# Kernel optimization log

Hardware: AMD Instinct MI355X
Metric: run time of the kernel (lower is better)

## Reference

```python
import jax, jax.numpy as jnp
import numpy as np

N, E, FN, FE, L, G = 4096, 16384, 16, 8, 128, 64
EPS = 1e-5


def setup_inputs() -> dict:
    key = jax.random.key(0)
    ks = iter(jax.random.split(key, 40))

    def lin_w(shape):
        return jax.random.normal(next(ks), shape, jnp.float32) * (1.0 / np.sqrt(shape[0]))

    d = {}
    d["x"] = jax.random.normal(next(ks), (N, FN), jnp.float32)
    d["edge_attr"] = jax.random.normal(next(ks), (E, FE), jnp.float32)
    d["edge_index"] = jax.random.randint(next(ks), (2, E), 0, N)
    d["batch"] = jnp.sort(jax.random.randint(next(ks), (N,), 0, G))
    for i, (cin, cout) in enumerate([(FN, 32), (32, 64), (64, 128)], 1):
        d[f"We{i}"] = lin_w((FE, cin * cout))          # edge_fc weight
        d[f"be{i}"] = jnp.zeros((cin * cout,), jnp.float32)
        d[f"bias{i}"] = jnp.zeros((cout,), jnp.float32)
        d[f"Wr{i}"] = lin_w((cin, cout))               # res_fc weight
        d[f"br{i}"] = jnp.zeros((cout,), jnp.float32)
        d[f"bn_g{i}"] = jnp.ones((cout,), jnp.float32)
        d[f"bn_b{i}"] = jnp.zeros((cout,), jnp.float32)
        d[f"a{i}"] = jnp.float32(0.25)                  # PReLU slope
    d["Wi"] = lin_w((128, 128)); d["bi"] = jnp.zeros((128,), jnp.float32)
    d["Wj"] = lin_w((128, 128)); d["bj"] = jnp.zeros((128,), jnp.float32)
    d["Wfc"] = lin_w((128, 2 * L)); d["bfc"] = jnp.zeros((2 * L,), jnp.float32)
    return d


def _ecc(x, src, dst, norm, edge_attr, We, be, bias, Wr, br, cout, cin):
    # dynamically generated per-edge filter: [E, out, in]
    theta = (edge_attr @ We + be).reshape(E, cout, cin)
    # gather source features, per-edge matvec, degree-normalize (norm_j)
    msg = norm[src][:, None] * jnp.einsum('eoi,ei->eo', theta, x[src])
    # scatter-add into destination nodes + bias + residual linear
    return jax.ops.segment_sum(msg, dst, num_segments=N) + bias + x @ Wr + br


def _bn(x, g, b):
    m = x.mean(0)
    v = x.var(0)  # biased variance, as torch BN training normalization
    return (x - m) * jax.lax.rsqrt(v + EPS) * g + b


def _prelu(x, a):
    return jnp.where(x >= 0, x, a * x)


def reference(x, edge_attr, edge_index, batch,
              We1, be1, bias1, Wr1, br1, bn_g1, bn_b1, a1,
              We2, be2, bias2, Wr2, br2, bn_g2, bn_b2, a2,
              We3, be3, bias3, Wr3, br3, bn_g3, bn_b3, a3,
              Wi, bi, Wj, bj, Wfc, bfc):
    src, dst = edge_index[0], edge_index[1]
    deg = jax.ops.segment_sum(jnp.ones((E,), x.dtype), src, num_segments=N)
    norm = jnp.where(deg > 0, 1.0 / deg, 0.0)

    h = _ecc(x, src, dst, norm, edge_attr, We1, be1, bias1, Wr1, br1, 32, FN)
    h = _prelu(_bn(h, bn_g1, bn_b1), a1)
    h = _ecc(h, src, dst, norm, edge_attr, We2, be2, bias2, Wr2, br2, 64, 32)
    h = _prelu(_bn(h, bn_g2, bn_b2), a2)
    h = _ecc(h, src, dst, norm, edge_attr, We3, be3, bias3, Wr3, br3, 128, 64)
    h = _prelu(_bn(h, bn_g3, bn_b3), a3)

    # gated attention pooling (GGS-NN eq. 7), scatter-sum per graph
    gates = jax.nn.sigmoid(h @ Wi + bi)
    feats = jnp.tanh(h @ Wj + bj)
    pooled = jnp.tanh(jax.ops.segment_sum(gates * feats, batch, num_segments=G))

    z = pooled @ Wfc + bfc  # [G, 2L]
    return z[:, :L], z[:, L:]
```

## Files before the change

kernel.cpp:

```cpp
#include <hip/hip_runtime.h>
#include <math.h>

#define NN 4096
#define NE 16384
#define NG 64

#define OFF_DEG   0
#define OFF_H1    4096
#define OFF_H2    135168
#define OFF_H3    397312
#define OFF_ST1   921600
#define OFF_ST2   921664
#define OFF_ST3   921792
#define OFF_POOL  922048
#define OFF_WC1   930240
#define OFF_WC2   934848
#define OFF_WC3   953280
#define OFF_Y     1027008
#define ZERO_FLOATS 930240

__device__ __forceinline__ void tr_wcat(const float* We, const float* be,
                                        float* Wcat, int CIN, int COUT, int t) {
    int nine = 9 * COUT;
    int i = t / nine; int r = t - i * nine;
    int f = r / COUT; int o = r - f * COUT;
    Wcat[t] = (f < 8) ? We[f * CIN * COUT + o * CIN + i] : be[o * CIN + i];
}

__global__ __launch_bounds__(256) void k_prep(
    const float* __restrict__ We1, const float* __restrict__ be1,
    const float* __restrict__ We2, const float* __restrict__ be2,
    const float* __restrict__ We3, const float* __restrict__ be3,
    const int* __restrict__ ei, float* __restrict__ ws)
{
    int t = blockIdx.x * 256 + threadIdx.x;
    if (t < 4608)  { tr_wcat(We1, be1, ws + OFF_WC1, 16, 32, t); return; }
    t -= 4608;
    if (t < 18432) { tr_wcat(We2, be2, ws + OFF_WC2, 32, 64, t); return; }
    t -= 18432;
    if (t < 73728) { tr_wcat(We3, be3, ws + OFF_WC3, 64, 128, t); return; }
    t -= 73728;
    if (t < NE)    { atomicAdd(&ws[OFF_DEG + ei[t]], 1.0f); }
}

template<int K>
__global__ __launch_bounds__(256) void k_proj(
    const float* __restrict__ A,
    const float* __restrict__ B,
    const float* __restrict__ deg,
    float* __restrict__ Y, int Ncols)
{
    __shared__ float sA[K][68];
    __shared__ float sB[K][68];
    const int tid = threadIdx.x;
    const int m0 = blockIdx.x * 64;
    const int n0 = blockIdx.y * 64;

    for (int t = tid; t < 64 * K; t += 256) {
        int m = t / K, i = t - m * K;
        sA[i][m] = A[(m0 + m) * K + i];
    }
    for (int t = tid; t < 64 * K; t += 256) {
        int i = t / 64, n = t - i * 64;
        int col = n0 + n;
        sB[i][n] = (col < Ncols) ? B[i * Ncols + col] : 0.f;
    }
    __syncthreads();

    const int tn = tid % 16, tm = tid / 16;
    float acc[4][4] = {{0.f}};
#pragma unroll 8
    for (int i = 0; i < K; ++i) {
        float4 a = *(const float4*)&sA[i][tm * 4];
        float4 b = *(const float4*)&sB[i][tn * 4];
        acc[0][0] += a.x * b.x; acc[0][1] += a.x * b.y; acc[0][2] += a.x * b.z; acc[0][3] += a.x * b.w;
        acc[1][0] += a.y * b.x; acc[1][1] += a.y * b.y; acc[1][2] += a.y * b.z; acc[1][3] += a.y * b.w;
        acc[2][0] += a.z * b.x; acc[2][1] += a.z * b.y; acc[2][2] += a.z * b.z; acc[2][3] += a.z * b.w;
        acc[3][0] += a.w * b.x; acc[3][1] += a.w * b.y; acc[3][2] += a.w * b.z; acc[3][3] += a.w * b.w;
    }

#pragma unroll
    for (int mm = 0; mm < 4; ++mm) {
        int m = m0 + tm * 4 + mm;
        float d = deg[m];
        float nrm = d > 0.f ? 1.f / d : 0.f;
#pragma unroll
        for (int nn = 0; nn < 4; ++nn) {
            int col = n0 + tn * 4 + nn;
            if (col < Ncols) Y[(size_t)m * Ncols + col] = acc[mm][nn] * nrm;
        }
    }
}

template<int COUT>
__global__ __launch_bounds__(256) void k_egather(
    const float* __restrict__ Y, const float* __restrict__ eattr,
    const int* __restrict__ ei, float* __restrict__ h)
{
    int idx = blockIdx.x * 256 + threadIdx.x;
    int e = idx / COUT;
    int o = idx - e * COUT;
    int src = ei[e], dst = ei[NE + e];
    const float* y = Y + (size_t)src * (9 * COUT);
    const float* ea = eattr + e * 8;
    float acc = y[8 * COUT + o];
#pragma unroll
    for (int f = 0; f < 8; ++f) acc += ea[f] * y[f * COUT + o];
    atomicAdd(&h[dst * COUT + o], acc);
}

template<int CIN, int COUT, int KN>
__global__ __launch_bounds__(256) void k_node(
    const float* __restrict__ xin, const float* __restrict__ Wr,
    const float* __restrict__ br, const float* __restrict__ bias,
    float* __restrict__ h, float* __restrict__ st)
{
    constexpr int NL = 256 / COUT;
    constexpr int NB = NL * KN;
    constexpr int CINP = CIN | 1;
    __shared__ float sWr[CIN * COUT];
    __shared__ float sX[NB * CINP];
    __shared__ float sred[256];
    const int tid = threadIdx.x;
    const int nbase = blockIdx.x * NB;

    for (int t = tid; t < CIN * COUT; t += 256) sWr[t] = Wr[t];
    for (int t = tid; t < NB * CIN; t += 256) {
        int r = t / CIN, i = t - r * CIN;
        sX[r * CINP + i] = xin[(nbase + r) * CIN + i];
    }
    __syncthreads();

    const int o = tid % COUT;
    const int nl = tid / COUT;
    const float addc = bias[o] + br[o];
    float sum = 0.f, sumsq = 0.f;
    for (int k = 0; k < KN; ++k) {
        int r = nl * KN + k;
        float a = addc;
        for (int i = 0; i < CIN; ++i)
            a += sX[r * CINP + i] * sWr[i * COUT + o];
        int gi = (nbase + r) * COUT + o;
        float hv = h[gi] + a;
        h[gi] = hv;
        sum += hv; sumsq += hv * hv;
    }
    sred[tid] = sum;
    __syncthreads();
    if (tid < COUT) {
        float s = 0.f;
        for (int g2 = 0; g2 < NL; ++g2) s += sred[g2 * COUT + tid];
        atomicAdd(&st[tid], s);
    }
    __syncthreads();
    sred[tid] = sumsq;
    __syncthreads();
    if (tid < COUT) {
        float s = 0.f;
        for (int g2 = 0; g2 < NL; ++g2) s += sred[g2 * COUT + tid];
        atomicAdd(&st[COUT + tid], s);
    }
}

template<int COUT>
__global__ __launch_bounds__(256) void k_bn(
    float* __restrict__ h, const float* __restrict__ st,
    const float* __restrict__ g, const float* __restrict__ b,
    const float* __restrict__ a)
{
    int idx = blockIdx.x * 256 + threadIdx.x;
    int o = idx % COUT;
    float mean = st[o] * (1.f / NN);
    float var = st[COUT + o] * (1.f / NN) - mean * mean;
    var = fmaxf(var, 0.f);
    float inv = rsqrtf(var + 1e-5f);
    float v = (h[idx] - mean) * inv * g[o] + b[o];
    h[idx] = v >= 0.f ? v : a[0] * v;
}

__global__ __launch_bounds__(256) void k_pool(
    const float* __restrict__ h3, const int* __restrict__ batch,
    const float* __restrict__ Wi, const float* __restrict__ bi,
    const float* __restrict__ Wj, const float* __restrict__ bj,
    float* __restrict__ pooled)
{
    constexpr int KN = 8, NB = 16;
    __shared__ float sH[NB * 128];
    __shared__ int sB[NB];
    const int tid = threadIdx.x;
    const int nbase = blockIdx.x * NB;
    for (int t = tid; t < NB * 128; t += 256) sH[t] = h3[nbase * 128 + t];
    if (tid < NB) sB[tid] = batch[nbase + tid];
    __syncthreads();

    const int o = tid % 128, nl = tid / 128;
    float gacc[KN], facc[KN];
#pragma unroll
    for (int k = 0; k < KN; ++k) { gacc[k] = 0.f; facc[k] = 0.f; }
    for (int i = 0; i < 128; ++i) {
        float wi = Wi[i * 128 + o], wj = Wj[i * 128 + o];
#pragma unroll
        for (int k = 0; k < KN; ++k) {
            float hv = sH[(nl * KN + k) * 128 + i];
            gacc[k] += hv * wi;
            facc[k] += hv * wj;
        }
    }
    float bio = bi[o], bjo = bj[o];
#pragma unroll
    for (int k = 0; k < KN; ++k) {
        int r = nl * KN + k;
        float gate = 1.f / (1.f + expf(-(gacc[k] + bio)));
        float feat = tanhf(facc[k] + bjo);
        atomicAdd(&pooled[sB[r] * 128 + o], gate * feat);
    }
}

__global__ __launch_bounds__(256) void k_final(
    const float* __restrict__ pooled, const float* __restrict__ Wfc,
    const float* __restrict__ bfc, float* __restrict__ out)
{
    __shared__ float sP[128];
    const int g = blockIdx.x, c = threadIdx.x;
    if (c < 128) sP[c] = tanhf(pooled[g * 128 + c]);
    __syncthreads();
    float z = bfc[c];
    for (int i = 0; i < 128; ++i) z += sP[i] * Wfc[i * 256 + c];
    int oidx = (c < 128) ? (g * 128 + c) : (NG * 128 + g * 128 + (c - 128));
    out[oidx] = z;
}

extern "C" void kernel_launch(void* const* d_in, const int* in_sizes, int n_in,
                              void* d_out, int out_size, void* d_ws, size_t ws_size,
                              hipStream_t stream)
{
    (void)in_sizes; (void)n_in; (void)out_size; (void)ws_size;
    const float* x     = (const float*)d_in[0];
    const float* eattr = (const float*)d_in[1];
    const int*   ei    = (const int*)d_in[2];
    const int*   batch = (const int*)d_in[3];
    const float* We1 = (const float*)d_in[4];
    const float* be1 = (const float*)d_in[5];
    const float* bias1 = (const float*)d_in[6];
    const float* Wr1 = (const float*)d_in[7];
    const float* br1 = (const float*)d_in[8];
    const float* bg1 = (const float*)d_in[9];
    const float* bb1 = (const float*)d_in[10];
    const float* a1  = (const float*)d_in[11];
    const float* We2 = (const float*)d_in[12];
    const float* be2 = (const float*)d_in[13];
    const float* bias2 = (const float*)d_in[14];
    const float* Wr2 = (const float*)d_in[15];
    const float* br2 = (const float*)d_in[16];
    const float* bg2 = (const float*)d_in[17];
    const float* bb2 = (const float*)d_in[18];
    const float* a2  = (const float*)d_in[19];
    const float* We3 = (const float*)d_in[20];
    const float* be3 = (const float*)d_in[21];
    const float* bias3 = (const float*)d_in[22];
    const float* Wr3 = (const float*)d_in[23];
    const float* br3 = (const float*)d_in[24];
    const float* bg3 = (const float*)d_in[25];
    const float* bb3 = (const float*)d_in[26];
    const float* a3  = (const float*)d_in[27];
    const float* Wi  = (const float*)d_in[28];
    const float* bi  = (const float*)d_in[29];
    const float* Wj  = (const float*)d_in[30];
    const float* bj  = (const float*)d_in[31];
    const float* Wfc = (const float*)d_in[32];
    const float* bfc = (const float*)d_in[33];
    float* ws  = (float*)d_ws;
    float* out = (float*)d_out;

    hipMemsetAsync(d_ws, 0, (size_t)ZERO_FLOATS * sizeof(float), stream);
    k_prep<<<442, 256, 0, stream>>>(We1, be1, We2, be2, We3, be3, ei, ws);

    k_proj<16><<<dim3(64, 5), 256, 0, stream>>>(x, ws + OFF_WC1, ws + OFF_DEG, ws + OFF_Y, 288);
    k_egather<32><<<NE * 32 / 256, 256, 0, stream>>>(ws + OFF_Y, eattr, ei, ws + OFF_H1);
    k_node<16, 32, 8><<<NN / 64, 256, 0, stream>>>(x, Wr1, br1, bias1, ws + OFF_H1, ws + OFF_ST1);
    k_bn<32><<<NN * 32 / 256, 256, 0, stream>>>(ws + OFF_H1, ws + OFF_ST1, bg1, bb1, a1);

    k_proj<32><<<dim3(64, 9), 256, 0, stream>>>(ws + OFF_H1, ws + OFF_WC2, ws + OFF_DEG, ws + OFF_Y, 576);
    k_egather<64><<<NE * 64 / 256, 256, 0, stream>>>(ws + OFF_Y, eattr, ei, ws + OFF_H2);
    k_node<32, 64, 8><<<NN / 32, 256, 0, stream>>>(ws + OFF_H1, Wr2, br2, bias2, ws + OFF_H2, ws + OFF_ST2);
    k_bn<64><<<NN * 64 / 256, 256, 0, stream>>>(ws + OFF_H2, ws + OFF_ST2, bg2, bb2, a2);

    k_proj<64><<<dim3(64, 18), 256, 0, stream>>>(ws + OFF_H2, ws + OFF_WC3, ws + OFF_DEG, ws + OFF_Y, 1152);
    k_egather<128><<<NE * 128 / 256, 256, 0, stream>>>(ws + OFF_Y, eattr, ei, ws + OFF_H3);
    k_node<64, 128, 8><<<NN / 16, 256, 0, stream>>>(ws + OFF_H2, Wr3, br3, bias3, ws + OFF_H3, ws + OFF_ST3);
    k_bn<128><<<NN * 128 / 256, 256, 0, stream>>>(ws + OFF_H3, ws + OFF_ST3, bg3, bb3, a3);

    k_pool<<<NN / 16, 256, 0, stream>>>(ws + OFF_H3, batch, Wi, bi, Wj, bj, ws + OFF_POOL);
    k_final<<<NG, 256, 0, stream>>>(ws + OFF_POOL, Wfc, bfc, out);
}
```

Before: 255.9 us.

## Fold residual linear into projection GEMM and fuse BN+PReLU into consumers

Appends the residual weight Wr as extra columns of the per-layer projection GEMM, so h is initialised with x@Wr+bias+br before edge scatter, which removes the separate node kernel. BatchNorm normalisation and PReLU are applied on load in the next layer's projection and in pooling, replacing the standalone BN kernels with a lighter stats-only pass. Degree normalisation moves into the edge gather, which now handles four channels per thread with float4 loads. This cuts kernel launches and full passes over h, and shrinks the zeroed workspace. The cost is that the edge gather still issues scalar atomics and extra per-element affine work in the loaders.

```diff
diff --git a/kernel.cpp b/kernel.cpp
--- a/kernel.cpp
+++ b/kernel.cpp
@@ -6,64 +6,84 @@
 #define NG 64
 
 #define OFF_DEG   0
-#define OFF_H1    4096
-#define OFF_H2    135168
-#define OFF_H3    397312
-#define OFF_ST1   921600
-#define OFF_ST2   921664
-#define OFF_ST3   921792
-#define OFF_POOL  922048
-#define OFF_WC1   930240
-#define OFF_WC2   934848
-#define OFF_WC3   953280
-#define OFF_Y     1027008
-#define ZERO_FLOATS 930240
-
-__device__ __forceinline__ void tr_wcat(const float* We, const float* be,
-                                        float* Wcat, int CIN, int COUT, int t) {
-    int nine = 9 * COUT;
-    int i = t / nine; int r = t - i * nine;
-    int f = r / COUT; int o = r - f * COUT;
-    Wcat[t] = (f < 8) ? We[f * CIN * COUT + o * CIN + i] : be[o * CIN + i];
+#define OFF_ST1   4096
+#define OFF_ST2   4160
+#define OFF_ST3   4288
+#define OFF_POOL  4544
+#define ZERO_FLOATS 12736
+#define OFF_H1    12736
+#define OFF_H2    143808
+#define OFF_H3    405952
+#define OFF_WX1   930240
+#define OFF_WX2   935360
+#define OFF_WX3   955840
+#define OFF_Y     1037760
+
+__device__ __forceinline__ void build_wext(const float* We, const float* be,
+                                           const float* Wr, float* Wx,
+                                           int CIN, int C, int t) {
+    int NC = 10 * C;
+    int i = t / NC; int col = t - i * NC;
+    float v;
+    if (col < 8 * C)      { int f = col / C, o = col - f * C; v = We[f * CIN * C + o * CIN + i]; }
+    else if (col < 9 * C) { int o = col - 8 * C;              v = be[o * CIN + i]; }
+    else                  { int o = col - 9 * C;              v = Wr[i * C + o]; }
+    Wx[t] = v;
 }
 
 __global__ __launch_bounds__(256) void k_prep(
-    const float* __restrict__ We1, const float* __restrict__ be1,
-    const float* __restrict__ We2, const float* __restrict__ be2,
-    const float* __restrict__ We3, const float* __restrict__ be3,
+    const float* __restrict__ We1, const float* __restrict__ be1, const float* __restrict__ Wr1,
+    const float* __restrict__ We2, const float* __restrict__ be2, const float* __restrict__ Wr2,
+    const float* __restrict__ We3, const float* __restrict__ be3, const float* __restrict__ Wr3,
     const int* __restrict__ ei, float* __restrict__ ws)
 {
     int t = blockIdx.x * 256 + threadIdx.x;
-    if (t < 4608)  { tr_wcat(We1, be1, ws + OFF_WC1, 16, 32, t); return; }
-    t -= 4608;
-    if (t < 18432) { tr_wcat(We2, be2, ws + OFF_WC2, 32, 64, t); return; }
-    t -= 18432;
-    if (t < 73728) { tr_wcat(We3, be3, ws + OFF_WC3, 64, 128, t); return; }
-    t -= 73728;
+    if (t < 5120)  { build_wext(We1, be1, Wr1, ws + OFF_WX1, 16, 32, t); return; }
+    t -= 5120;
+    if (t < 20480) { build_wext(We2, be2, Wr2, ws + OFF_WX2, 32, 64, t); return; }
+    t -= 20480;
+    if (t < 81920) { build_wext(We3, be3, Wr3, ws + OFF_WX3, 64, 128, t); return; }
+    t -= 81920;
     if (t < NE)    { atomicAdd(&ws[OFF_DEG + ei[t]], 1.0f); }
 }
 
-template<int K>
+template<int K, int C, bool BN>
 __global__ __launch_bounds__(256) void k_proj(
-    const float* __restrict__ A,
-    const float* __restrict__ B,
-    const float* __restrict__ deg,
-    float* __restrict__ Y, int Ncols)
-{
+    const float* __restrict__ A, const float* __restrict__ Bw,
+    const float* __restrict__ st, const float* __restrict__ bg,
+    const float* __restrict__ bb, const float* __restrict__ alpha,
+    const float* __restrict__ bias, const float* __restrict__ br,
+    float* __restrict__ Y, float* __restrict__ h)
+{
+    constexpr int NC = 10 * C;
     __shared__ float sA[K][68];
     __shared__ float sB[K][68];
+    __shared__ float sS[K], sT[K];
     const int tid = threadIdx.x;
     const int m0 = blockIdx.x * 64;
     const int n0 = blockIdx.y * 64;
 
+    float al = 0.f;
+    if constexpr (BN) {
+        if (tid < K) {
+            float mean = st[tid] * (1.f / NN);
+            float var  = st[K + tid] * (1.f / NN) - mean * mean;
+            var = fmaxf(var, 0.f);
+            float s = rsqrtf(var + 1e-5f) * bg[tid];
+            sS[tid] = s; sT[tid] = bb[tid] - mean * s;
+        }
+        al = alpha[0];
+        __syncthreads();
+    }
     for (int t = tid; t < 64 * K; t += 256) {
         int m = t / K, i = t - m * K;
-        sA[i][m] = A[(m0 + m) * K + i];
+        float v = A[(m0 + m) * K + i];
+        if constexpr (BN) { v = sS[i] * v + sT[i]; v = v >= 0.f ? v : al * v; }
+        sA[i][m] = v;
     }
     for (int t = tid; t < 64 * K; t += 256) {
         int i = t / 64, n = t - i * 64;
-        int col = n0 + n;
-        sB[i][n] = (col < Ncols) ? B[i * Ncols + col] : 0.f;
+        sB[i][n] = Bw[i * NC + n0 + n];
     }
     __syncthreads();
 
@@ -79,117 +99,125 @@
         acc[3][0] += a.w * b.x; acc[3][1] += a.w * b.y; acc[3][2] += a.w * b.z; acc[3][3] += a.w * b.w;
     }
 
-#pragma unroll
-    for (int mm = 0; mm < 4; ++mm) {
-        int m = m0 + tm * 4 + mm;
-        float d = deg[m];
-        float nrm = d > 0.f ? 1.f / d : 0.f;
-#pragma unroll
-        for (int nn = 0; nn < 4; ++nn) {
-            int col = n0 + tn * 4 + nn;
-            if (col < Ncols) Y[(size_t)m * Ncols + col] = acc[mm][nn] * nrm;
-        }
-    }
-}
-
-template<int COUT>
+    if (n0 + 64 <= 9 * C) {
+#pragma unroll
+        for (int mm = 0; mm < 4; ++mm) {
+            int m = m0 + tm * 4 + mm;
+            float4 v = make_float4(acc[mm][0], acc[mm][1], acc[mm][2], acc[mm][3]);
+            *(float4*)&Y[(size_t)m * (9 * C) + n0 + tn * 4] = v;
+        }
+    } else if (n0 >= 9 * C) {
+        int o = n0 - 9 * C + tn * 4;
+        float4 add = *(const float4*)&bias[o];
+        float4 ad2 = *(const float4*)&br[o];
+#pragma unroll
+        for (int mm = 0; mm < 4; ++mm) {
+            int m = m0 + tm * 4 + mm;
+            float4 v = make_float4(acc[mm][0] + add.x + ad2.x, acc[mm][1] + add.y + ad2.y,
+                                   acc[mm][2] + add.z + ad2.z, acc[mm][3] + add.w + ad2.w);
+            *(float4*)&h[(size_t)m * C + o] = v;
+        }
+    } else {
+#pragma unroll
+        for (int mm = 0; mm < 4; ++mm) {
+            int m = m0 + tm * 4 + mm;
+#pragma unroll
+            for (int nn = 0; nn < 4; ++nn) {
+                int col = n0 + tn * 4 + nn;
+                if (col < 9 * C) Y[(size_t)m * (9 * C) + col] = acc[mm][nn];
+                else { int o = col - 9 * C; h[(size_t)m * C + o] = acc[mm][nn] + bias[o] + br[o]; }
+            }
+        }
+    }
+}
+
+template<int C>
 __global__ __launch_bounds__(256) void k_egather(
     const float* __restrict__ Y, const float* __restrict__ eattr,
-    const int* __restrict__ ei, float* __restrict__ h)
-{
+    const int* __restrict__ ei, const float* __restrict__ deg,
+    float* __restrict__ h)
+{
+    constexpr int Q = C / 4;
     int idx = blockIdx.x * 256 + threadIdx.x;
-    int e = idx / COUT;
-    int o = idx - e * COUT;
+    int e = idx / Q;
+    int q = idx - e * Q;
     int src = ei[e], dst = ei[NE + e];
-    const float* y = Y + (size_t)src * (9 * COUT);
+    float d = deg[src];
+    float nrm = d > 0.f ? 1.f / d : 0.f;
+    const float4* y = (const float4*)(Y + (size_t)src * (9 * C));
     const float* ea = eattr + e * 8;
-    float acc = y[8 * COUT + o];
-#pragma unroll
-    for (int f = 0; f < 8; ++f) acc += ea[f] * y[f * COUT + o];
-    atomicAdd(&h[dst * COUT + o], acc);
-}
-
-template<int CIN, int COUT, int KN>
-__global__ __launch_bounds__(256) void k_node(
-    const float* __restrict__ xin, const float* __restrict__ Wr,
-    const float* __restrict__ br, const float* __restrict__ bias,
-    float* __restrict__ h, float* __restrict__ st)
-{
-    constexpr int NL = 256 / COUT;
-    constexpr int NB = NL * KN;
-    constexpr int CINP = CIN | 1;
-    __shared__ float sWr[CIN * COUT];
-    __shared__ float sX[NB * CINP];
+    float4 acc = y[8 * Q + q];
+#pragma unroll
+    for (int f = 0; f < 8; ++f) {
+        float4 yf = y[f * Q + q];
+        float w = ea[f];
+        acc.x += w * yf.x; acc.y += w * yf.y; acc.z += w * yf.z; acc.w += w * yf.w;
+    }
+    float* hp = h + (size_t)dst * C + q * 4;
+    atomicAdd(hp + 0, acc.x * nrm);
+    atomicAdd(hp + 1, acc.y * nrm);
+    atomicAdd(hp + 2, acc.z * nrm);
+    atomicAdd(hp + 3, acc.w * nrm);
+}
+
+template<int C>
+__global__ __launch_bounds__(256) void k_bnstat(const float* __restrict__ h, float* __restrict__ st)
+{
+    constexpr int NL = 256 / C;
     __shared__ float sred[256];
     const int tid = threadIdx.x;
-    const int nbase = blockIdx.x * NB;
-
-    for (int t = tid; t < CIN * COUT; t += 256) sWr[t] = Wr[t];
-    for (int t = tid; t < NB * CIN; t += 256) {
-        int r = t / CIN, i = t - r * CIN;
-        sX[r * CINP + i] = xin[(nbase + r) * CIN + i];
-    }
-    __syncthreads();
-
-    const int o = tid % COUT;
-    const int nl = tid / COUT;
-    const float addc = bias[o] + br[o];
-    float sum = 0.f, sumsq = 0.f;
-    for (int k = 0; k < KN; ++k) {
-        int r = nl * KN + k;
-        float a = addc;
-        for (int i = 0; i < CIN; ++i)
-            a += sX[r * CINP + i] * sWr[i * COUT + o];
-        int gi = (nbase + r) * COUT + o;
-        float hv = h[gi] + a;
-        h[gi] = hv;
-        sum += hv; sumsq += hv * hv;
+    const int o = tid % C, nl = tid / C;
+    const int rbase = blockIdx.x * 64;
+    float sum = 0.f, sq = 0.f;
+    for (int r = nl; r < 64; r += NL) {
+        float v = h[(size_t)(rbase + r) * C + o];
+        sum += v; sq += v * v;
     }
     sred[tid] = sum;
     __syncthreads();
-    if (tid < COUT) {
+    if (tid < C) {
         float s = 0.f;
-        for (int g2 = 0; g2 < NL; ++g2) s += sred[g2 * COUT + tid];
+        for (int g2 = 0; g2 < NL; ++g2) s += sred[g2 * C + tid];
         atomicAdd(&st[tid], s);
     }
     __syncthreads();
-    sred[tid] = sumsq;
-    __syncthreads();
-    if (tid < COUT) {
+    sred[tid] = sq;
+    __syncthreads();
+    if (tid < C) {
         float s = 0.f;
-        for (int g2 = 0; g2 < NL; ++g2) s += sred[g2 * COUT + tid];
-        atomicAdd(&st[COUT + tid], s);
-    }
-}
-
-template<int COUT>
-__global__ __launch_bounds__(256) void k_bn(
-    float* __restrict__ h, const float* __restrict__ st,
-    const float* __restrict__ g, const float* __restrict__ b,
-    const float* __restrict__ a)
-{
-    int idx = blockIdx.x * 256 + threadIdx.x;
-    int o = idx % COUT;
-    float mean = st[o] * (1.f / NN);
-    float var = st[COUT + o] * (1.f / NN) - mean * mean;
-    var = fmaxf(var, 0.f);
-    float inv = rsqrtf(var + 1e-5f);
-    float v = (h[idx] - mean) * inv * g[o] + b[o];
-    h[idx] = v >= 0.f ? v : a[0] * v;
+        for (int g2 = 0; g2 < NL; ++g2) s += sred[g2 * C + tid];
+        atomicAdd(&st[C + tid], s);
+    }
 }
 
 __global__ __launch_bounds__(256) void k_pool(
     const float* __restrict__ h3, const int* __restrict__ batch,
+    const float* __restrict__ st, const float* __restrict__ bg,
+    const float* __restrict__ bb, const float* __restrict__ alpha,
     const float* __restrict__ Wi, const float* __restrict__ bi,
     const float* __restrict__ Wj, const float* __restrict__ bj,
     float* __restrict__ pooled)
 {
     constexpr int KN = 8, NB = 16;
     __shared__ float sH[NB * 128];
+    __shared__ float sS[128], sT[128];
     __shared__ int sB[NB];
     const int tid = threadIdx.x;
     const int nbase = blockIdx.x * NB;
-    for (int t = tid; t < NB * 128; t += 256) sH[t] = h3[nbase * 128 + t];
+    if (tid < 128) {
+        float mean = st[tid] * (1.f / NN);
+        float var  = st[128 + tid] * (1.f / NN) - mean * mean;
+        var = fmaxf(var, 0.f);
+        float s = rsqrtf(var + 1e-5f) * bg[tid];
+        sS[tid] = s; sT[tid] = bb[tid] - mean * s;
+    }
+    float al = alpha[0];
+    __syncthreads();
+    for (int t = tid; t < NB * 128; t += 256) {
+        int i = t % 128;
+        float v = sS[i] * h3[(size_t)nbase * 128 + t] + sT[i];
+        sH[t] = v >= 0.f ? v : al * v;
+    }
     if (tid < NB) sB[tid] = batch[nbase + tid];
     __syncthreads();
 
@@ -273,23 +301,24 @@
     float* out = (float*)d_out;
 
     hipMemsetAsync(d_ws, 0, (size_t)ZERO_FLOATS * sizeof(float), stream);
-    k_prep<<<442, 256, 0, stream>>>(We1, be1, We2, be2, We3, be3, ei, ws);
-
-    k_proj<16><<<dim3(64, 5), 256, 0, stream>>>(x, ws + OFF_WC1, ws + OFF_DEG, ws + OFF_Y, 288);
-    k_egather<32><<<NE * 32 / 256, 256, 0, stream>>>(ws + OFF_Y, eattr, ei, ws + OFF_H1);
-    k_node<16, 32, 8><<<NN / 64, 256, 0, stream>>>(x, Wr1, br1, bias1, ws + OFF_H1, ws + OFF_ST1);
-    k_bn<32><<<NN * 32 / 256, 256, 0, stream>>>(ws + OFF_H1, ws + OFF_ST1, bg1, bb1, a1);
-
-    k_proj<32><<<dim3(64, 9), 256, 0, stream>>>(ws + OFF_H1, ws + OFF_WC2, ws + OFF_DEG, ws + OFF_Y, 576);
-    k_egather<64><<<NE * 64 / 256, 256, 0, stream>>>(ws + OFF_Y, eattr, ei, ws + OFF_H2);
-    k_node<32, 64, 8><<<NN / 32, 256, 0, stream>>>(ws + OFF_H1, Wr2, br2, bias2, ws + OFF_H2, ws + OFF_ST2);
-    k_bn<64><<<NN * 64 / 256, 256, 0, stream>>>(ws + OFF_H2, ws + OFF_ST2, bg2, bb2, a2);
-
-    k_proj<64><<<dim3(64, 18), 256, 0, stream>>>(ws + OFF_H2, ws + OFF_WC3, ws + OFF_DEG, ws + OFF_Y, 1152);
-    k_egather<128><<<NE * 128 / 256, 256, 0, stream>>>(ws + OFF_Y, eattr, ei, ws + OFF_H3);
-    k_node<64, 128, 8><<<NN / 16, 256, 0, stream>>>(ws + OFF_H2, Wr3, br3, bias3, ws + OFF_H3, ws + OFF_ST3);
-    k_bn<128><<<NN * 128 / 256, 256, 0, stream>>>(ws + OFF_H3, ws + OFF_ST3, bg3, bb3, a3);
-
-    k_pool<<<NN / 16, 256, 0, stream>>>(ws + OFF_H3, batch, Wi, bi, Wj, bj, ws + OFF_POOL);
+    k_prep<<<484, 256, 0, stream>>>(We1, be1, Wr1, We2, be2, Wr2, We3, be3, Wr3, ei, ws);
+
+    k_proj<16, 32, false><<<dim3(64, 5), 256, 0, stream>>>(
+        x, ws + OFF_WX1, nullptr, nullptr, nullptr, nullptr, bias1, br1, ws + OFF_Y, ws + OFF_H1);
+    k_egather<32><<<NE * 8 / 256, 256, 0, stream>>>(ws + OFF_Y, eattr, ei, ws + OFF_DEG, ws + OFF_H1);
+    k_bnstat<32><<<64, 256, 0, stream>>>(ws + OFF_H1, ws + OFF_ST1);
+
+    k_proj<32, 64, true><<<dim3(64, 10), 256, 0, stream>>>(
+        ws + OFF_H1, ws + OFF_WX2, ws + OFF_ST1, bg1, bb1, a1, bias2, br2, ws + OFF_Y, ws + OFF_H2);
+    k_egather<64><<<NE * 16 / 256, 256, 0, stream>>>(ws + OFF_Y, eattr, ei, ws + OFF_DEG, ws + OFF_H2);
+    k_bnstat<64><<<64, 256, 0, stream>>>(ws + OFF_H2, ws + OFF_ST2);
+
+    k_proj<64, 128, true><<<dim3(64, 20), 256, 0, stream>>>(
+        ws + OFF_H2, ws + OFF_WX3, ws + OFF_ST2, bg2, bb2, a2, bias3, br3, ws + OFF_Y, ws + OFF_H3);
+    k_egather<128><<<NE * 32 / 256, 256, 0, stream>>>(ws + OFF_Y, eattr, ei, ws + OFF_DEG, ws + OFF_H3);
+    k_bnstat<128><<<64, 256, 0, stream>>>(ws + OFF_H3, ws + OFF_ST3);
+
+    k_pool<<<NN / 16, 256, 0, stream>>>(ws + OFF_H3, batch, ws + OFF_ST3, bg3, bb3, a3,
+                                        Wi, bi, Wj, bj, ws + OFF_POOL);
     k_final<<<NG, 256, 0, stream>>>(ws + OFF_POOL, Wfc, bfc, out);
 }
```

Result: slower. 274.4 us (+7.2%).
